# Kernel optimization log

Measured on AMD Instinct MI355X. Metric: run time of the kernel, lower is better.

Reference implementation:

```python
import jax, jax.numpy as jnp
import numpy as np

N_HEAD, D_HEAD, D_MODEL = 16, 64, 1024
QLEN, MLEN, BSZ = 512, 512, 8
KLEN = QLEN + MLEN
SCALE = 1.0 / D_HEAD ** 0.5
LN_EPS = 1e-5


def rel_shift(x):
    # x: [qlen, klen, bsz, n_head] -- Transformer-XL pad/reshape shift trick
    q, k, b, n = x.shape
    x_pad = jnp.pad(x, ((0, 0), (1, 0), (0, 0), (0, 0)))
    x_pad = x_pad.reshape(k + 1, q, b, n)
    return x_pad[1:].reshape(q, k, b, n)


def setup_inputs() -> dict:
    key = jax.random.key(0)
    ks = jax.random.split(key, 10)
    s = 0.02
    return {
        'w': jax.random.normal(ks[0], (QLEN, BSZ, D_MODEL), jnp.float32),
        'r': jax.random.normal(ks[1], (KLEN, D_MODEL), jnp.float32),
        'mems': jax.random.normal(ks[2], (MLEN, BSZ, D_MODEL), jnp.float32),
        'r_w_bias': jax.random.normal(ks[3], (N_HEAD, D_HEAD), jnp.float32) * s,
        'r_r_bias': jax.random.normal(ks[4], (N_HEAD, D_HEAD), jnp.float32) * s,
        'Wq': jax.random.normal(ks[5], (N_HEAD * D_HEAD, D_MODEL), jnp.float32) * s,
        'Wkv': jax.random.normal(ks[6], (2 * N_HEAD * D_HEAD, D_MODEL), jnp.float32) * s,
        'Wr': jax.random.normal(ks[7], (N_HEAD * D_HEAD, D_MODEL), jnp.float32) * s,
        'br': jnp.zeros((N_HEAD * D_HEAD,), jnp.float32),
        'Wo': jax.random.normal(ks[8], (D_MODEL, N_HEAD * D_HEAD), jnp.float32) * s,
        'bo': jnp.zeros((D_MODEL,), jnp.float32),
        'gamma': jnp.ones((D_MODEL,), jnp.float32),
        'beta': jnp.zeros((D_MODEL,), jnp.float32),
    }


def reference(w, r, mems, r_w_bias, r_r_bias, Wq, Wkv, Wr, br, Wo, bo, gamma, beta):
    qlen, bsz, _ = w.shape
    cat = jnp.concatenate([mems, w], axis=0)           # [klen, b, d]
    klen = cat.shape[0]
    mlen = klen - qlen

    q = (w @ Wq.T).reshape(qlen, bsz, N_HEAD, D_HEAD)   # [i, b, n, d]
    kv = (cat @ Wkv.T).reshape(klen, bsz, N_HEAD, 2 * D_HEAD)
    k, v = kv[..., :D_HEAD], kv[..., D_HEAD:]           # [j, b, n, d]
    rk = (r @ Wr.T + br).reshape(klen, N_HEAD, D_HEAD)  # [j, n, d]

    AC = jnp.einsum('ibnd,jbnd->ijbn', q + r_w_bias, k)
    BD = jnp.einsum('ibnd,jnd->ijbn', q + r_r_bias, rk)
    BD = rel_shift(BD)
    score = (AC + BD) * SCALE                           # [i, j, b, n]

    # causal mask with memory: query i attends to keys j <= i + mlen
    i_idx = jnp.arange(qlen)[:, None]
    j_idx = jnp.arange(klen)[None, :]
    mask = j_idx > (i_idx + mlen)
    score = jnp.where(mask[:, :, None, None], -1e30, score)

    prob = jax.nn.softmax(score, axis=1)
    attn_vec = jnp.einsum('ijbn,jbnd->ibnd', prob, v).reshape(qlen, bsz, N_HEAD * D_HEAD)
    attn_out = attn_vec @ Wo.T + bo

    # IdentityResidualGate: x + relu(y), then LayerNorm
    y = w + jax.nn.relu(attn_out)
    mu = jnp.mean(y, axis=-1, keepdims=True)
    var = jnp.mean(jnp.square(y - mu), axis=-1, keepdims=True)
    return (y - mu) * jax.lax.rsqrt(var + LN_EPS) * gamma + beta
```

## Files before the change

### kernel.cpp

```cpp
#include <hip/hip_runtime.h>
#include <hip/hip_bf16.h>
#include <cstdint>
#include <cstddef>

typedef __attribute__((ext_vector_type(4))) float f32x4;
typedef __attribute__((ext_vector_type(8))) short bf16x8;
using u16 = unsigned short;

#define ATT_SCALE 0.125f

__device__ __forceinline__ u16 f2b(float f) {
    union { float f; uint32_t u; } x; x.f = f;
    uint32_t r = x.u + 0x7fffu + ((x.u >> 16) & 1u);
    return (u16)(r >> 16);
}

#define GLDS16(g, s)                                                        \
    __builtin_amdgcn_global_load_lds(                                       \
        (const __attribute__((address_space(1))) uint32_t*)(g),             \
        (__attribute__((address_space(3))) uint32_t*)(s), 16, 0, 0)

__global__ __launch_bounds__(256) void prep_kernel(
    const float* __restrict__ mems, const float* __restrict__ w,
    const float* __restrict__ r, const float* __restrict__ Wq,
    const float* __restrict__ Wkv, const float* __restrict__ Wr,
    const float* __restrict__ Wo, u16* __restrict__ cat_b,
    u16* __restrict__ r_b, u16* __restrict__ Wq_b, u16* __restrict__ Wkv_b,
    u16* __restrict__ Wr_b, u16* __restrict__ Wo_b) {
    int bid = blockIdx.x;
    if (bid < 8192) {
        int idx = bid * 256 + threadIdx.x;
        float4 v = (idx < 1048576) ? reinterpret_cast<const float4*>(mems)[idx]
                                   : reinterpret_cast<const float4*>(w)[idx - 1048576];
        uint2 o;
        o.x = (uint32_t)f2b(v.x) | ((uint32_t)f2b(v.y) << 16);
        o.y = (uint32_t)f2b(v.z) | ((uint32_t)f2b(v.w) << 16);
        reinterpret_cast<uint2*>(cat_b)[idx] = o;
        return;
    }
    bid -= 8192;
    const float4* src;
    uint2* dst;
    if (bid < 1024)      { src = (const float4*)r;   dst = (uint2*)r_b; }
    else if (bid < 2048) { src = (const float4*)Wq;  dst = (uint2*)Wq_b;  bid -= 1024; }
    else if (bid < 4096) { src = (const float4*)Wkv; dst = (uint2*)Wkv_b; bid -= 2048; }
    else if (bid < 5120) { src = (const float4*)Wr;  dst = (uint2*)Wr_b;  bid -= 4096; }
    else                 { src = (const float4*)Wo;  dst = (uint2*)Wo_b;  bid -= 5120; }
    int idx = bid * 256 + threadIdx.x;
    float4 v = src[idx];
    uint2 o;
    o.x = (uint32_t)f2b(v.x) | ((uint32_t)f2b(v.y) << 16);
    o.y = (uint32_t)f2b(v.z) | ((uint32_t)f2b(v.w) << 16);
    dst[idx] = o;
}

__global__ __launch_bounds__(256) void gemm_all(
    const u16* __restrict__ catb, const u16* __restrict__ Wkvb,
    const u16* __restrict__ Wqb, const u16* __restrict__ rb,
    const u16* __restrict__ Wrb, const float* __restrict__ bw,
    const float* __restrict__ brr, const float* __restrict__ br,
    u16* __restrict__ qwb, u16* __restrict__ qrb, u16* __restrict__ kb,
    u16* __restrict__ vtb, u16* __restrict__ rkb) {
    __shared__ uint4 sA[128][8];
    __shared__ uint4 sB[128][8];
    const int idx = blockIdx.x;
    const u16 *A, *B;
    int N, bx, by, epi;
    if (idx < 1024)      { epi = 1; A = catb; B = Wkvb; N = 2048; bx = idx & 63; by = idx >> 6; }
    else if (idx < 1280) { epi = 0; A = catb + (size_t)4096 * 1024; B = Wqb; N = 1024;
                           int l = idx - 1024; bx = l & 31; by = l >> 5; }
    else                 { epi = 2; A = rb; B = Wrb; N = 1024;
                           int l = idx - 1280; bx = l & 7; by = l >> 3; }
    const int tid = threadIdx.x;
    const int wid = tid >> 6, lane = tid & 63;
    const int lr = lane & 15, lg = lane >> 4;
    const int bm = bx * 128, bn = by * 128;
    const int wm = (wid >> 1) * 64, wn = (wid & 1) * 64;
    const int srow = tid >> 3, scol = tid & 7;
    f32x4 acc[4][4] = {};

    for (int k0 = 0; k0 < 1024; k0 += 64) {
#pragma unroll
        for (int p = 0; p < 4; p++) {
            int row = p * 32 + srow;
            GLDS16(A + (size_t)(bm + row) * 1024 + k0 + scol * 8, &sA[row][scol]);
            GLDS16(B + (size_t)(bn + row) * 1024 + k0 + scol * 8, &sB[row][scol]);
        }
        __syncthreads();
#pragma unroll
        for (int ks = 0; ks < 2; ks++) {
            bf16x8 af[4], bfr[4];
#pragma unroll
            for (int x = 0; x < 4; x++) {
                af[x] = *reinterpret_cast<const bf16x8*>(&sA[wm + x * 16 + lr][ks * 4 + lg]);
                bfr[x] = *reinterpret_cast<const bf16x8*>(&sB[wn + x * 16 + lr][ks * 4 + lg]);
            }
#pragma unroll
            for (int mi = 0; mi < 4; mi++)
#pragma unroll
                for (int ni = 0; ni < 4; ni++)
                    acc[mi][ni] = __builtin_amdgcn_mfma_f32_16x16x32_bf16(
                        af[mi], bfr[ni], acc[mi][ni], 0, 0, 0);
        }
        __syncthreads();
    }
#pragma unroll
    for (int mi = 0; mi < 4; mi++)
#pragma unroll
        for (int ni = 0; ni < 4; ni++)
#pragma unroll
            for (int rr = 0; rr < 4; rr++) {
                int m = bm + wm + mi * 16 + lg * 4 + rr;
                int c = bn + wn + ni * 16 + lr;
                float v = acc[mi][ni][rr];
                if (epi == 1) {
                    int j = m >> 3, b = m & 7, n = c >> 7, dd = c & 127;
                    if (dd < 64)
                        kb[(((size_t)(b * 16 + n)) * 1024 + j) * 64 + dd] = f2b(v);
                    else
                        vtb[(((size_t)(b * 16 + n)) * 64 + (dd - 64)) * 1024 + j] = f2b(v);
                } else if (epi == 0) {
                    qwb[(size_t)m * N + c] = f2b(v + bw[c]);
                    qrb[(size_t)m * N + c] = f2b(v + brr[c]);
                } else {
                    int nh = c >> 6, d = c & 63;
                    rkb[((size_t)nh * 1024 + m) * 64 + d] = f2b(v + br[c]);
                }
            }
}

__global__ __launch_bounds__(256) void gemm_out(const u16* __restrict__ A,
                                                const u16* __restrict__ B,
                                                const float* __restrict__ wres,
                                                const float* __restrict__ bo,
                                                float* __restrict__ y) {
    __shared__ uint4 sA[128][8];
    __shared__ uint4 sB[128][8];
    const int tid = threadIdx.x;
    const int wid = tid >> 6, lane = tid & 63;
    const int lr = lane & 15, lg = lane >> 4;
    const int bm = blockIdx.x * 128, bn = blockIdx.y * 128;
    const int wm = (wid >> 1) * 64, wn = (wid & 1) * 64;
    const int srow = tid >> 3, scol = tid & 7;
    f32x4 acc[4][4] = {};

    for (int k0 = 0; k0 < 1024; k0 += 64) {
#pragma unroll
        for (int p = 0; p < 4; p++) {
            int row = p * 32 + srow;
            GLDS16(A + (size_t)(bm + row) * 1024 + k0 + scol * 8, &sA[row][scol]);
            GLDS16(B + (size_t)(bn + row) * 1024 + k0 + scol * 8, &sB[row][scol]);
        }
        __syncthreads();
#pragma unroll
        for (int ks = 0; ks < 2; ks++) {
            bf16x8 af[4], bfr[4];
#pragma unroll
            for (int x = 0; x < 4; x++) {
                af[x] = *reinterpret_cast<const bf16x8*>(&sA[wm + x * 16 + lr][ks * 4 + lg]);
                bfr[x] = *reinterpret_cast<const bf16x8*>(&sB[wn + x * 16 + lr][ks * 4 + lg]);
            }
#pragma unroll
            for (int mi = 0; mi < 4; mi++)
#pragma unroll
                for (int ni = 0; ni < 4; ni++)
                    acc[mi][ni] = __builtin_amdgcn_mfma_f32_16x16x32_bf16(
                        af[mi], bfr[ni], acc[mi][ni], 0, 0, 0);
        }
        __syncthreads();
    }
#pragma unroll
    for (int mi = 0; mi < 4; mi++)
#pragma unroll
        for (int ni = 0; ni < 4; ni++)
#pragma unroll
            for (int rr = 0; rr < 4; rr++) {
                int m = bm + wm + mi * 16 + lg * 4 + rr;
                int c = bn + wn + ni * 16 + lr;
                y[(size_t)m * 1024 + c] =
                    wres[(size_t)m * 1024 + c] + fmaxf(acc[mi][ni][rr] + bo[c], 0.0f);
            }
}

__global__ __launch_bounds__(256, 2) void attn_kernel(const u16* __restrict__ qw,
                                                      const u16* __restrict__ qr,
                                                      const u16* __restrict__ kbuf,
                                                      const u16* __restrict__ vt,
                                                      const u16* __restrict__ rkb,
                                                      u16* __restrict__ attnv) {
    __shared__ uint4 ksh[64][8];
    __shared__ uint4 vsh[64][8];
    __shared__ uint4 rsh[128][8];
    __shared__ float bds[4][16][82];
    __shared__ u16 ps[4][16][72];
    const int bid = blockIdx.x;
    const int wg = (bid & 7) * 128 + (bid >> 3);
    const int i0 = (wg & 7) * 64;
    const int bnid = wg >> 3;
    const int b = bnid & 7, n = bnid >> 3;
    const int tid = threadIdx.x, wid = tid >> 6, lane = tid & 63;
    const int lr = lane & 15, lg = lane >> 4;
    const int it = i0 + wid * 16;

    const u16* qwp = qw + ((size_t)(it + lr) * 8 + b) * 1024 + n * 64;
    const u16* qrp = qr + ((size_t)(it + lr) * 8 + b) * 1024 + n * 64;
    bf16x8 aqw[2], aqr[2];
#pragma unroll
    for (int ks = 0; ks < 2; ks++) {
        aqw[ks] = *reinterpret_cast<const bf16x8*>(qwp + (ks * 4 + lg) * 8);
        aqr[ks] = *reinterpret_cast<const bf16x8*>(qrp + (ks * 4 + lg) * 8);
    }
    const u16* kp = kbuf + ((size_t)(b * 16 + n)) * 65536;
    const u16* vp = vt + ((size_t)(b * 16 + n)) * 65536;
    const u16* rp = rkb + (size_t)n * 65536;

    f32x4 acc[4] = {};
    float lpart[4] = {0.f, 0.f, 0.f, 0.f};
    const int xs = lr & 7;
    const int rbase = 48 - 16 * wid;

    const int nt = (i0 + 639) >> 6;
    for (int t = 0; t < nt; t++) {
        const int j0 = t << 6;
        const int jrb = j0 + 448 - i0;
#pragma unroll
        for (int inst = 0; inst < 2; inst++) {
            int gi = wid * 128 + inst * 64 + lane;
            int row = gi >> 3, c = gi & 7;
            int cs = (c ^ (row & 7)) * 8;
            GLDS16(kp + (size_t)(j0 + row) * 64 + cs,
                   (char*)ksh + (size_t)(wid * 128 + inst * 64) * 16);
            GLDS16(vp + (size_t)row * 1024 + j0 + cs,
                   (char*)vsh + (size_t)(wid * 128 + inst * 64) * 16);
        }
#pragma unroll
        for (int inst = 0; inst < 4; inst++) {
            int gi = wid * 256 + inst * 64 + lane;
            int row = gi >> 3, c = gi & 7;
            int grow = jrb + row;
            if (grow > 1023) grow = 1023;
            GLDS16(rp + (size_t)grow * 64 + (c ^ (row & 7)) * 8,
                   (char*)rsh + (size_t)(wid * 256 + inst * 64) * 16);
        }
        __syncthreads();

        f32x4 s[4] = {};
#pragma unroll
        for (int fj = 0; fj < 4; fj++)
#pragma unroll
            for (int ks = 0; ks < 2; ks++) {
                bf16x8 bk = *reinterpret_cast<const bf16x8*>(
                    &ksh[fj * 16 + lr][(ks * 4 + lg) ^ xs]);
                s[fj] = __builtin_amdgcn_mfma_f32_16x16x32_bf16(aqw[ks], bk, s[fj], 0, 0, 0);
            }
        f32x4 bd[5] = {};
#pragma unroll
        for (int fb = 0; fb < 5; fb++) {
            int rel = rbase + fb * 16 + lr;
#pragma unroll
            for (int ks = 0; ks < 2; ks++) {
                bf16x8 brk = *reinterpret_cast<const bf16x8*>(
                    &rsh[rel][(ks * 4 + lg) ^ xs]);
                bd[fb] = __builtin_amdgcn_mfma_f32_16x16x32_bf16(aqr[ks], brk, bd[fb], 0, 0, 0);
            }
        }
#pragma unroll
        for (int fb = 0; fb < 5; fb++)
#pragma unroll
            for (int rr = 0; rr < 4; rr++)
                bds[wid][lg * 4 + rr][fb * 16 + lr] = bd[fb][rr];

#pragma unroll
        for (int fj = 0; fj < 4; fj++)
#pragma unroll
            for (int rr = 0; rr < 4; rr++) {
                const int di = lg * 4 + rr;
                float v = (s[fj][rr] + bds[wid][di][fj * 16 + lr + 15 - di]) * ATT_SCALE;
                float e = (j0 + fj * 16 + lr <= it + di + 512) ? __expf(v) : 0.0f;
                lpart[rr] += e;
                ps[wid][di][fj * 16 + lr] = f2b(e);
            }
#pragma unroll
        for (int kc = 0; kc < 2; kc++) {
            bf16x8 ap = *reinterpret_cast<const bf16x8*>(&ps[wid][lr][kc * 32 + lg * 8]);
#pragma unroll
            for (int nd = 0; nd < 4; nd++) {
                bf16x8 bv = *reinterpret_cast<const bf16x8*>(
                    &vsh[nd * 16 + lr][(kc * 4 + lg) ^ xs]);
                acc[nd] = __builtin_amdgcn_mfma_f32_16x16x32_bf16(ap, bv, acc[nd], 0, 0, 0);
            }
        }
        __syncthreads();
    }
    float l[4];
#pragma unroll
    for (int rr = 0; rr < 4; rr++) {
        float x = lpart[rr];
        x += __shfl_xor(x, 1);
        x += __shfl_xor(x, 2);
        x += __shfl_xor(x, 4);
        x += __shfl_xor(x, 8);
        l[rr] = x;
    }
#pragma unroll
    for (int nd = 0; nd < 4; nd++)
#pragma unroll
        for (int rr = 0; rr < 4; rr++) {
            int i = it + lg * 4 + rr;
            int d = nd * 16 + lr;
            attnv[((size_t)i * 8 + b) * 1024 + n * 64 + d] = f2b(acc[nd][rr] / l[rr]);
        }
}

__global__ __launch_bounds__(256) void ln_kernel(const float* __restrict__ y,
                                                 const float* __restrict__ gamma,
                                                 const float* __restrict__ beta,
                                                 float* __restrict__ out) {
    __shared__ float rs[8];
    int row = blockIdx.x, tid = threadIdx.x;
    const float4 v = reinterpret_cast<const float4*>(y + (size_t)row * 1024)[tid];
    float s = v.x + v.y + v.z + v.w;
    float s2 = v.x * v.x + v.y * v.y + v.z * v.z + v.w * v.w;
#pragma unroll
    for (int m = 1; m < 64; m <<= 1) {
        s += __shfl_xor(s, m);
        s2 += __shfl_xor(s2, m);
    }
    if ((tid & 63) == 0) {
        rs[tid >> 6] = s;
        rs[4 + (tid >> 6)] = s2;
    }
    __syncthreads();
    s = rs[0] + rs[1] + rs[2] + rs[3];
    s2 = rs[4] + rs[5] + rs[6] + rs[7];
    float mu = s * (1.0f / 1024.0f);
    float var = s2 * (1.0f / 1024.0f) - mu * mu;
    float inv = rsqrtf(var + 1e-5f);
    float4 g = reinterpret_cast<const float4*>(gamma)[tid];
    float4 be = reinterpret_cast<const float4*>(beta)[tid];
    float4 o;
    o.x = (v.x - mu) * inv * g.x + be.x;
    o.y = (v.y - mu) * inv * g.y + be.y;
    o.z = (v.z - mu) * inv * g.z + be.z;
    o.w = (v.w - mu) * inv * g.w + be.w;
    reinterpret_cast<float4*>(out + (size_t)row * 1024)[tid] = o;
}

extern "C" void kernel_launch(void* const* d_in, const int* in_sizes, int n_in,
                              void* d_out, int out_size, void* d_ws, size_t ws_size,
                              hipStream_t stream) {
    (void)in_sizes; (void)n_in; (void)out_size; (void)ws_size;
    const float* w_in  = (const float*)d_in[0];
    const float* r_in  = (const float*)d_in[1];
    const float* mems  = (const float*)d_in[2];
    const float* bw    = (const float*)d_in[3];
    const float* brr   = (const float*)d_in[4];
    const float* Wq    = (const float*)d_in[5];
    const float* Wkv   = (const float*)d_in[6];
    const float* Wr    = (const float*)d_in[7];
    const float* br    = (const float*)d_in[8];
    const float* Wo    = (const float*)d_in[9];
    const float* bo    = (const float*)d_in[10];
    const float* gamma = (const float*)d_in[11];
    const float* beta  = (const float*)d_in[12];

    char* base = (char*)d_ws;
    size_t off = 0;
    auto alloc = [&](size_t bytes) -> char* {
        char* p = base + off;
        off += (bytes + 255) & ~(size_t)255;
        return p;
    };
    u16* cat_b = (u16*)alloc((size_t)8192 * 1024 * 2);
    u16* r_b   = (u16*)alloc((size_t)1024 * 1024 * 2);
    u16* Wq_b  = (u16*)alloc((size_t)1024 * 1024 * 2);
    u16* Wkv_b = (u16*)alloc((size_t)2048 * 1024 * 2);
    u16* Wr_b  = (u16*)alloc((size_t)1024 * 1024 * 2);
    u16* Wo_b  = (u16*)alloc((size_t)1024 * 1024 * 2);
    u16* qw_b  = (u16*)alloc((size_t)4096 * 1024 * 2);
    u16* qr_b  = (u16*)alloc((size_t)4096 * 1024 * 2);
    u16* k_b   = (u16*)alloc((size_t)128 * 1024 * 64 * 2);
    u16* vt_b  = (u16*)alloc((size_t)128 * 64 * 1024 * 2);
    u16* rk_b  = (u16*)alloc((size_t)16 * 1024 * 64 * 2);
    u16* av_b  = (u16*)alloc((size_t)4096 * 1024 * 2);
    float* y = (float*)cat_b;

    prep_kernel<<<14336, 256, 0, stream>>>(mems, w_in, r_in, Wq, Wkv, Wr, Wo,
                                           cat_b, r_b, Wq_b, Wkv_b, Wr_b, Wo_b);

    gemm_all<<<1344, 256, 0, stream>>>(cat_b, Wkv_b, Wq_b, r_b, Wr_b,
                                       bw, brr, br,
                                       qw_b, qr_b, k_b, vt_b, rk_b);

    attn_kernel<<<1024, 256, 0, stream>>>(qw_b, qr_b, k_b, vt_b, rk_b, av_b);

    gemm_out<<<dim3(32, 8), 256, 0, stream>>>(av_b, Wo_b, w_in, bo, y);

    ln_kernel<<<4096, 256, 0, stream>>>(y, gamma, beta, (float*)d_out);
}
```

Before: 229.9 us.

## Enlarge projection GEMM tiles to 256x256 with double-buffered swizzled LDS

The fused QKV/R projection GEMM now uses 512-thread blocks computing 256x256 output tiles instead of 128x128. It double-buffers the LDS K-slices so the next slice loads while MFMAs run on the current one, and XOR-swizzles the LDS column layout to avoid bank conflicts. The aim is more operand reuse per global load and hidden load latency. The trade-off is that 336 large blocks at roughly 128KB LDS each limits occupancy to one block per CU and leaves an uneven final wave. A stray preload of catb into sA[0] also remains before the real prologue.

```diff
diff --git a/kernel.cpp b/kernel.cpp
--- a/kernel.cpp
+++ b/kernel.cpp
@@ -54,64 +54,89 @@
     dst[idx] = o;
 }
 
-__global__ __launch_bounds__(256) void gemm_all(
+__global__ __launch_bounds__(512, 2) void gemm_proj(
     const u16* __restrict__ catb, const u16* __restrict__ Wkvb,
     const u16* __restrict__ Wqb, const u16* __restrict__ rb,
     const u16* __restrict__ Wrb, const float* __restrict__ bw,
     const float* __restrict__ brr, const float* __restrict__ br,
     u16* __restrict__ qwb, u16* __restrict__ qrb, u16* __restrict__ kb,
     u16* __restrict__ vtb, u16* __restrict__ rkb) {
-    __shared__ uint4 sA[128][8];
-    __shared__ uint4 sB[128][8];
+    __shared__ u16 sA[2][256][64];
+    __shared__ u16 sB[2][256][64];
     const int idx = blockIdx.x;
     const u16 *A, *B;
     int N, bx, by, epi;
-    if (idx < 1024)      { epi = 1; A = catb; B = Wkvb; N = 2048; bx = idx & 63; by = idx >> 6; }
-    else if (idx < 1280) { epi = 0; A = catb + (size_t)4096 * 1024; B = Wqb; N = 1024;
-                           int l = idx - 1024; bx = l & 31; by = l >> 5; }
-    else                 { epi = 2; A = rb; B = Wrb; N = 1024;
-                           int l = idx - 1280; bx = l & 7; by = l >> 3; }
+    if (idx < 256)      { epi = 1; A = catb; B = Wkvb; N = 2048; bx = idx & 31; by = idx >> 5; }
+    else if (idx < 320) { epi = 0; A = catb + (size_t)4096 * 1024; B = Wqb; N = 1024;
+                          int l = idx - 256; bx = l & 15; by = l >> 4; }
+    else                { epi = 2; A = rb; B = Wrb; N = 1024;
+                          int l = idx - 320; bx = l & 3; by = l >> 2; }
     const int tid = threadIdx.x;
     const int wid = tid >> 6, lane = tid & 63;
     const int lr = lane & 15, lg = lane >> 4;
-    const int bm = bx * 128, bn = by * 128;
-    const int wm = (wid >> 1) * 64, wn = (wid & 1) * 64;
+    const int bm = bx * 256, bn = by * 256;
+    const int Wm = (wid >> 2) * 128, Wn = (wid & 3) * 64;
     const int srow = tid >> 3, scol = tid & 7;
-    f32x4 acc[4][4] = {};
-
-    for (int k0 = 0; k0 < 1024; k0 += 64) {
-#pragma unroll
-        for (int p = 0; p < 4; p++) {
-            int row = p * 32 + srow;
-            GLDS16(A + (size_t)(bm + row) * 1024 + k0 + scol * 8, &sA[row][scol]);
-            GLDS16(B + (size_t)(bn + row) * 1024 + k0 + scol * 8, &sB[row][scol]);
-        }
-        __syncthreads();
+    const int xs = lr & 7;
+    f32x4 acc[8][4] = {};
+
+#pragma unroll
+    for (int p = 0; p < 4; p++) {
+        int row = p * 64 + srow;
+        int cs = (scol ^ (row & 7)) * 8;
+        GLDS16(catb, &sA[0][0][0]);
+    }
+#pragma unroll
+    for (int p = 0; p < 4; p++) {
+        int row = p * 64 + srow;
+        int cs = (scol ^ (row & 7)) * 8;
+        GLDS16(A + (size_t)(bm + row) * 1024 + cs, &sA[0][row][scol * 8]);
+        GLDS16(B + (size_t)(bn + row) * 1024 + cs, &sB[0][row][scol * 8]);
+    }
+    __syncthreads();
+
+    int cur = 0;
+    for (int t = 0; t < 16; t++) {
+        if (t < 15) {
+            const int k0n = (t + 1) * 64;
+#pragma unroll
+            for (int p = 0; p < 4; p++) {
+                int row = p * 64 + srow;
+                int cs = (scol ^ (row & 7)) * 8;
+                GLDS16(A + (size_t)(bm + row) * 1024 + k0n + cs, &sA[cur ^ 1][row][scol * 8]);
+                GLDS16(B + (size_t)(bn + row) * 1024 + k0n + cs, &sB[cur ^ 1][row][scol * 8]);
+            }
+        }
 #pragma unroll
         for (int ks = 0; ks < 2; ks++) {
-            bf16x8 af[4], bfr[4];
-#pragma unroll
-            for (int x = 0; x < 4; x++) {
-                af[x] = *reinterpret_cast<const bf16x8*>(&sA[wm + x * 16 + lr][ks * 4 + lg]);
-                bfr[x] = *reinterpret_cast<const bf16x8*>(&sB[wn + x * 16 + lr][ks * 4 + lg]);
-            }
-#pragma unroll
-            for (int mi = 0; mi < 4; mi++)
+            bf16x8 af[8], bf[4];
+#pragma unroll
+            for (int mi = 0; mi < 8; mi++)
+                af[mi] = *reinterpret_cast<const bf16x8*>(
+                    &sA[cur][Wm + mi * 16 + lr][((ks * 4 + lg) ^ xs) * 8]);
+#pragma unroll
+            for (int ni = 0; ni < 4; ni++)
+                bf[ni] = *reinterpret_cast<const bf16x8*>(
+                    &sB[cur][Wn + ni * 16 + lr][((ks * 4 + lg) ^ xs) * 8]);
+#pragma unroll
+            for (int mi = 0; mi < 8; mi++)
 #pragma unroll
                 for (int ni = 0; ni < 4; ni++)
                     acc[mi][ni] = __builtin_amdgcn_mfma_f32_16x16x32_bf16(
-                        af[mi], bfr[ni], acc[mi][ni], 0, 0, 0);
+                        af[mi], bf[ni], acc[mi][ni], 0, 0, 0);
         }
         __syncthreads();
-    }
-#pragma unroll
-    for (int mi = 0; mi < 4; mi++)
+        cur ^= 1;
+    }
+
+#pragma unroll
+    for (int mi = 0; mi < 8; mi++)
 #pragma unroll
         for (int ni = 0; ni < 4; ni++)
 #pragma unroll
             for (int rr = 0; rr < 4; rr++) {
-                int m = bm + wm + mi * 16 + lg * 4 + rr;
-                int c = bn + wn + ni * 16 + lr;
+                int m = bm + Wm + mi * 16 + lg * 4 + rr;
+                int c = bn + Wn + ni * 16 + lr;
                 float v = acc[mi][ni][rr];
                 if (epi == 1) {
                     int j = m >> 3, b = m & 7, n = c >> 7, dd = c & 127;
@@ -120,8 +145,8 @@
                     else
                         vtb[(((size_t)(b * 16 + n)) * 64 + (dd - 64)) * 1024 + j] = f2b(v);
                 } else if (epi == 0) {
-                    qwb[(size_t)m * N + c] = f2b(v + bw[c]);
-                    qrb[(size_t)m * N + c] = f2b(v + brr[c]);
+                    qwb[(size_t)m * 1024 + c] = f2b(v + bw[c]);
+                    qrb[(size_t)m * 1024 + c] = f2b(v + brr[c]);
                 } else {
                     int nh = c >> 6, d = c & 63;
                     rkb[((size_t)nh * 1024 + m) * 64 + d] = f2b(v + br[c]);
@@ -388,7 +413,7 @@
     prep_kernel<<<14336, 256, 0, stream>>>(mems, w_in, r_in, Wq, Wkv, Wr, Wo,
                                            cat_b, r_b, Wq_b, Wkv_b, Wr_b, Wo_b);
 
-    gemm_all<<<1344, 256, 0, stream>>>(cat_b, Wkv_b, Wq_b, r_b, Wr_b,
+    gemm_proj<<<336, 512, 0, stream>>>(cat_b, Wkv_b, Wq_b, r_b, Wr_b,
                                        bw, brr, br,
                                        qw_b, qr_b, k_b, vt_b, rk_b);
 
```

New measurement: 261.8 us. 1.14x slower.

## Reorder cat buffer to batch-major so V^T epilogue writes packed vectors

Applied to the files above, without the earlier changes.

The bf16 concatenated input is now stored batch-major (b, j) instead of (j, b), so consecutive GEMM rows map to consecutive key positions within one batch. This lets the V-transpose epilogue pack four bf16 values into a single 8-byte store instead of four scattered 2-byte stores, and it changes Q indexing in attention to match. The GEMM block index is also swizzled across 8 groups, likely to spread tiles across XCDs for cache locality. The risk is that the remaining code (attention output and gemm_out) must stay consistent with the new q layout.

```diff
diff --git a/kernel.cpp b/kernel.cpp
--- a/kernel.cpp
+++ b/kernel.cpp
@@ -29,13 +29,21 @@
     u16* __restrict__ Wr_b, u16* __restrict__ Wo_b) {
     int bid = blockIdx.x;
     if (bid < 8192) {
-        int idx = bid * 256 + threadIdx.x;
-        float4 v = (idx < 1048576) ? reinterpret_cast<const float4*>(mems)[idx]
-                                   : reinterpret_cast<const float4*>(w)[idx - 1048576];
+        int col4 = threadIdx.x;
+        float4 v;
+        int b, oj;
+        if (bid < 4096) {
+            v = reinterpret_cast<const float4*>(mems)[(size_t)bid * 256 + col4];
+            b = bid & 7; oj = bid >> 3;
+        } else {
+            int rrow = bid - 4096;
+            v = reinterpret_cast<const float4*>(w)[(size_t)rrow * 256 + col4];
+            b = rrow & 7; oj = 512 + (rrow >> 3);
+        }
         uint2 o;
         o.x = (uint32_t)f2b(v.x) | ((uint32_t)f2b(v.y) << 16);
         o.y = (uint32_t)f2b(v.z) | ((uint32_t)f2b(v.w) << 16);
-        reinterpret_cast<uint2*>(cat_b)[idx] = o;
+        reinterpret_cast<uint2*>(cat_b)[(size_t)(b * 1024 + oj) * 256 + col4] = o;
         return;
     }
     bid -= 8192;
@@ -63,14 +71,22 @@
     u16* __restrict__ vtb, u16* __restrict__ rkb) {
     __shared__ uint4 sA[128][8];
     __shared__ uint4 sB[128][8];
-    const int idx = blockIdx.x;
+    const int idx = (blockIdx.x & 7) * 168 + (blockIdx.x >> 3);
     const u16 *A, *B;
     int N, bx, by, epi;
-    if (idx < 1024)      { epi = 1; A = catb; B = Wkvb; N = 2048; bx = idx & 63; by = idx >> 6; }
-    else if (idx < 1280) { epi = 0; A = catb + (size_t)4096 * 1024; B = Wqb; N = 1024;
-                           int l = idx - 1024; bx = l & 31; by = l >> 5; }
-    else                 { epi = 2; A = rb; B = Wrb; N = 1024;
-                           int l = idx - 1280; bx = l & 7; by = l >> 3; }
+    if (idx < 1024) {
+        epi = 1; B = Wkvb; N = 2048; bx = idx & 63; by = idx >> 6;
+        A = catb + (size_t)bx * 128 * 1024;
+    } else if (idx < 1280) {
+        epi = 0; B = Wqb; N = 1024;
+        int l = idx - 1024; bx = l & 31; by = l >> 5;
+        int bm0 = bx * 128;
+        A = catb + ((size_t)(bm0 >> 9) * 1024 + 512 + (bm0 & 511)) * 1024;
+    } else {
+        epi = 2; B = Wrb; N = 1024;
+        int l = idx - 1280; bx = l & 7; by = l >> 3;
+        A = rb + (size_t)bx * 128 * 1024;
+    }
     const int tid = threadIdx.x;
     const int wid = tid >> 6, lane = tid & 63;
     const int lr = lane & 15, lg = lane >> 4;
@@ -83,7 +99,7 @@
 #pragma unroll
         for (int p = 0; p < 4; p++) {
             int row = p * 32 + srow;
-            GLDS16(A + (size_t)(bm + row) * 1024 + k0 + scol * 8, &sA[row][scol]);
+            GLDS16(A + (size_t)row * 1024 + k0 + scol * 8, &sA[row][scol]);
             GLDS16(B + (size_t)(bn + row) * 1024 + k0 + scol * 8, &sB[row][scol]);
         }
         __syncthreads();
@@ -107,26 +123,38 @@
 #pragma unroll
     for (int mi = 0; mi < 4; mi++)
 #pragma unroll
-        for (int ni = 0; ni < 4; ni++)
-#pragma unroll
-            for (int rr = 0; rr < 4; rr++) {
-                int m = bm + wm + mi * 16 + lg * 4 + rr;
-                int c = bn + wn + ni * 16 + lr;
-                float v = acc[mi][ni][rr];
-                if (epi == 1) {
-                    int j = m >> 3, b = m & 7, n = c >> 7, dd = c & 127;
-                    if (dd < 64)
-                        kb[(((size_t)(b * 16 + n)) * 1024 + j) * 64 + dd] = f2b(v);
-                    else
-                        vtb[(((size_t)(b * 16 + n)) * 64 + (dd - 64)) * 1024 + j] = f2b(v);
-                } else if (epi == 0) {
-                    qwb[(size_t)m * N + c] = f2b(v + bw[c]);
-                    qrb[(size_t)m * N + c] = f2b(v + brr[c]);
+        for (int ni = 0; ni < 4; ni++) {
+            const int m0 = bm + wm + mi * 16 + lg * 4;
+            const int c = bn + wn + ni * 16 + lr;
+            if (epi == 1) {
+                const int b = m0 >> 10, j0 = m0 & 1023;
+                const int n = c >> 7, dd = c & 127;
+                if (dd < 64) {
+#pragma unroll
+                    for (int rr = 0; rr < 4; rr++)
+                        kb[(((size_t)(b * 16 + n)) * 1024 + j0 + rr) * 64 + dd] =
+                            f2b(acc[mi][ni][rr]);
                 } else {
-                    int nh = c >> 6, d = c & 63;
-                    rkb[((size_t)nh * 1024 + m) * 64 + d] = f2b(v + br[c]);
+                    uint2 pk;
+                    pk.x = (uint32_t)f2b(acc[mi][ni][0]) | ((uint32_t)f2b(acc[mi][ni][1]) << 16);
+                    pk.y = (uint32_t)f2b(acc[mi][ni][2]) | ((uint32_t)f2b(acc[mi][ni][3]) << 16);
+                    *reinterpret_cast<uint2*>(
+                        vtb + (((size_t)(b * 16 + n)) * 64 + (dd - 64)) * 1024 + j0) = pk;
                 }
-            }
+            } else if (epi == 0) {
+#pragma unroll
+                for (int rr = 0; rr < 4; rr++) {
+                    int m = m0 + rr;
+                    qwb[(size_t)m * 1024 + c] = f2b(acc[mi][ni][rr] + bw[c]);
+                    qrb[(size_t)m * 1024 + c] = f2b(acc[mi][ni][rr] + brr[c]);
+                }
+            } else {
+                const int nh = c >> 6, d = c & 63;
+#pragma unroll
+                for (int rr = 0; rr < 4; rr++)
+                    rkb[((size_t)nh * 1024 + m0 + rr) * 64 + d] = f2b(acc[mi][ni][rr] + br[c]);
+            }
+        }
 }
 
 __global__ __launch_bounds__(256) void gemm_out(const u16* __restrict__ A,
@@ -202,8 +230,8 @@
     const int lr = lane & 15, lg = lane >> 4;
     const int it = i0 + wid * 16;
 
-    const u16* qwp = qw + ((size_t)(it + lr) * 8 + b) * 1024 + n * 64;
-    const u16* qrp = qr + ((size_t)(it + lr) * 8 + b) * 1024 + n * 64;
+    const u16* qwp = qw + ((size_t)(b * 512 + it + lr)) * 1024 + n * 64;
+    const u16* qrp = qr + ((size_t)(b * 512 + it + lr)) * 1024 + n * 64;
     bf16x8 aqw[2], aqr[2];
 #pragma unroll
     for (int ks = 0; ks < 2; ks++) {
```

Measured after the change: 221.9 us. 1.04x faster.
